# Optimization experiments

Measured on AMD Instinct MI355X. Metric: run time of the kernel, lower is better.

The kernel has to match this reference:

```python
import jax, jax.numpy as jnp
import numpy as np

IN_C = 256
INTER_C = 64  # in_c // k, k=4
B, H, W = 8, 32, 32
N_TERMS = 5   # numSeriesTerms; numTraceSamples = 1


def setup_inputs():
    key = jax.random.key(0)
    ks = jax.random.split(key, 10)
    s = 0.05
    return {
        "x": jax.random.normal(ks[0], (B, IN_C, H, W), jnp.float32),
        "Wq": jax.random.normal(ks[1], (INTER_C, IN_C), jnp.float32) * s,
        "bq": jax.random.normal(ks[2], (INTER_C,), jnp.float32) * s,
        "Wk": jax.random.normal(ks[3], (INTER_C, IN_C), jnp.float32) * s,
        "bk": jax.random.normal(ks[4], (INTER_C,), jnp.float32) * s,
        "Wc": jax.random.normal(ks[5], (2 * INTER_C,), jnp.float32) * s,
        "Wv": jax.random.normal(ks[6], (IN_C, IN_C), jnp.float32) * s,
        "bv": jax.random.normal(ks[7], (IN_C,), jnp.float32) * s,
        "gamma": jnp.full((1,), 0.5, jnp.float32),
        "u": jax.random.normal(ks[8], (B, IN_C, H, W), jnp.float32),
    }


def _attention(x, Wq, bq, Wk, bk, Wc, Wv, bv, gamma):
    # Attention_concat.forward. concat_conv is a bias-free linear map over the
    # channel concat, so energy[i,j] = <Wc[:ic], q_i> + <Wc[ic:], k_j> exactly.
    b, c, h, w = x.shape
    n = h * w
    xf = x.reshape(b, c, n)                                   # [B,C,N]
    q = jnp.einsum('oc,bcn->bon', Wq, xf) + bq[None, :, None]  # [B,ic,N]
    k = jnp.einsum('oc,bcn->bon', Wk, xf) + bk[None, :, None]  # [B,ic,N]
    ic = Wq.shape[0]
    eq = jnp.einsum('c,bcn->bn', Wc[:ic], q)                  # [B,N]
    ek = jnp.einsum('c,bcn->bn', Wc[ic:], k)                  # [B,N]
    attn = (eq[:, :, None] + ek[:, None, :]) / n              # energy/(H*W), [B,N,N]
    v = jnp.einsum('oc,bcn->bon', Wv, xf) + bv[None, :, None]  # [B,C,N]
    out = jnp.einsum('bcn,bnm->bcm', v, attn).reshape(b, c, h, w)
    return gamma * out + x


def _forward(x, Wq, bq, Wk, bk, Wc, Wv, bv, gamma, u):
    att = lambda z, g: _attention(z, Wq, bq, Wk, bk, Wc, Wv, bv, g)
    # turbulance_hook: runs under torch.no_grad and rescales gamma in-place
    res = att(x, gamma)
    turbu = att(x * 1.0000001, gamma)
    lip = jnp.linalg.norm(turbu - res) / jnp.linalg.norm(x * 1.0000001 - x)
    factor = jax.lax.stop_gradient(jnp.where(lip > 0.9, 0.9 / lip, 1.0))
    gamma_eff = gamma * factor
    Fx, vjp_fn = jax.vjp(lambda z: att(z, gamma_eff), x)
    # power_series_matrix_logarithm_trace: Hutchinson estimate of
    # tr(log(I+J)) ~= sum_j (-1)^{j+1}/j * u^T J^j u, 1 probe, 5 terms
    b = x.shape[0]
    uf = u.reshape(b, -1)
    vcur = u
    tr = jnp.zeros((b,), x.dtype)
    for j in range(1, N_TERMS + 1):
        vcur = vjp_fn(vcur)[0]                 # u^T J^j via repeated vjp
        dot = jnp.sum(vcur.reshape(b, -1) * uf, axis=1)
        tr = tr + ((-1.0) ** (j + 1) / j) * dot
    return x + Fx, tr


def reference(x, Wq, bq, Wk, bk, Wc, Wv, bv, gamma, u):
    return _forward(x, Wq, bq, Wk, bk, Wc, Wv, bv, gamma, u)
```

## Files before the change

kernel.cpp:

```cpp
#include <hip/hip_runtime.h>
#include <math.h>

#define NB 8
#define NC 256
#define NN 1024
#define NICH 64

#define WS_AQ    0
#define WS_AK    256
#define WS_MOM2  520
#define WS_SX    1024
#define WS_XE    3072
#define WS_XK    5120
#define WS_T1P   7424
#define WS_T2P   7488
#define WS_VSU   7680
#define WS_UE    9728
#define WS_VEU   11776
#define WS_CAQ   13824
#define WS_CAK   15872
#define WS_CUAK  17920
#define WS_STAT  20480
#define STAT_STRIDE 2560
#define ST_EK    1024
#define ST_SV    2048
#define ST_SVE   2304
#define WS_EQP2  57344
#define WS_EKP2  90112
#define WS_MAQP2 122880
#define WS_MAKP2 155648
#define WS_SX2P  188416
#define WS_UUP   188672
#define WS_WVB   188928

typedef short bf16x8 __attribute__((ext_vector_type(8)));
typedef float f32x4 __attribute__((ext_vector_type(4)));
union FragU { uint4 u; bf16x8 h; };

__device__ __forceinline__ float dot4(const float4& a, const float4& b) {
    return a.x * b.x + a.y * b.y + a.z * b.z + a.w * b.w;
}
__device__ __forceinline__ float sum4(const float4& a) {
    return a.x + a.y + a.z + a.w;
}
__device__ __forceinline__ unsigned int bf16lo(float v) {
    unsigned int u = __float_as_uint(v);
    return (u + 0x7FFFu + ((u >> 16) & 1u)) >> 16;
}
__device__ __forceinline__ unsigned int bf16hi(float v) {
    unsigned int u = __float_as_uint(v);
    return (u + 0x7FFFu + ((u >> 16) & 1u)) & 0xFFFF0000u;
}

__global__ void kA(const float* __restrict__ x, const float* __restrict__ u,
                   const float* __restrict__ Wq, const float* __restrict__ Wk,
                   const float* __restrict__ Wc, const float* __restrict__ Wv,
                   float* __restrict__ ws) {
    const int bid = blockIdx.x;
    const int t = threadIdx.x;
    __shared__ float tile[64][65];
    __shared__ float aql[64], akl[64];
    __shared__ float4 red_e[32][8], red_k[32][8], red_a[32][8], red_m[32][8];
    if (bid >= 256) {
        const int o0 = (bid - 256) * 64;
        const int cho = t >> 6, ol = t & 63;
        uint4* wvb4 = (uint4*)((unsigned int*)ws + WS_WVB);
        for (int p4 = 0; p4 < 4; ++p4) {
#pragma unroll 4
            for (int p = 0; p < 16; ++p) {
                int cl = p * 4 + cho;
                tile[cl][ol] = Wv[(size_t)(p4 * 64 + cl) * NC + o0 + ol];
            }
            __syncthreads();
#pragma unroll
            for (int i = 0; i < 2; ++i) {
                int idx2 = i * 256 + t;
                int o_l = idx2 >> 3, gg = idx2 & 7;
                int g = p4 * 8 + gg;
                int o = o0 + o_l;
                int s = g ^ (o & 7);
                uint4 outv;
                outv.x = bf16lo(tile[gg * 8 + 0][o_l]) | bf16hi(tile[gg * 8 + 1][o_l]);
                outv.y = bf16lo(tile[gg * 8 + 2][o_l]) | bf16hi(tile[gg * 8 + 3][o_l]);
                outv.z = bf16lo(tile[gg * 8 + 4][o_l]) | bf16hi(tile[gg * 8 + 5][o_l]);
                outv.w = bf16lo(tile[gg * 8 + 6][o_l]) | bf16hi(tile[gg * 8 + 7][o_l]);
                wvb4[(size_t)(bid - 256) * 2048 + o_l * 32 + s] = outv;
            }
            __syncthreads();
        }
        return;
    }
    const int b = bid >> 5, r = bid & 31;
    const int nq = r >> 2, chq = r & 3;
    if (t < 64) {
        const int c = chq * 64 + t;
        float a = 0.f, k = 0.f;
#pragma unroll 8
        for (int o = 0; o < 64; ++o) {
            a += Wc[o] * Wq[o * NC + c];
            k += Wc[64 + o] * Wk[o * NC + c];
        }
        aql[t] = a; akl[t] = k;
        if (nq == 0) { ws[WS_AQ + c] = a; ws[WS_AK + c] = k; }
    }
    __syncthreads();
    const int f4g = t & 31, sub = t >> 5;
    const float4* xb4 = (const float4*)(x + ((size_t)b * NC + chq * 64) * NN);
    const float4* ub4 = (const float4*)(u + ((size_t)b * NC + chq * 64) * NN);
    float4 eqp = {0.f, 0.f, 0.f, 0.f}, ekp = {0.f, 0.f, 0.f, 0.f};
    float4 map = {0.f, 0.f, 0.f, 0.f}, mkp = {0.f, 0.f, 0.f, 0.f};
#pragma unroll
    for (int i = 0; i < 8; ++i) {
        const int cl = sub * 8 + i;
        float4 xv = xb4[cl * 256 + nq * 32 + f4g];
        float4 uv = ub4[cl * 256 + nq * 32 + f4g];
        const float a = aql[cl], kk = akl[cl];
        eqp.x += a * xv.x;  eqp.y += a * xv.y;  eqp.z += a * xv.z;  eqp.w += a * xv.w;
        ekp.x += kk * xv.x; ekp.y += kk * xv.y; ekp.z += kk * xv.z; ekp.w += kk * xv.w;
        map.x += a * uv.x;  map.y += a * uv.y;  map.z += a * uv.z;  map.w += a * uv.w;
        mkp.x += kk * uv.x; mkp.y += kk * uv.y; mkp.z += kk * uv.z; mkp.w += kk * uv.w;
    }
    red_e[f4g][sub] = eqp; red_k[f4g][sub] = ekp;
    red_a[f4g][sub] = map; red_m[f4g][sub] = mkp;
    __syncthreads();
    if (t < 32) {
        float4 e = red_e[t][0], k = red_k[t][0], a = red_a[t][0], m = red_m[t][0];
#pragma unroll
        for (int s2 = 1; s2 < 8; ++s2) {
            float4 v;
            v = red_e[t][s2]; e.x += v.x; e.y += v.y; e.z += v.z; e.w += v.w;
            v = red_k[t][s2]; k.x += v.x; k.y += v.y; k.z += v.z; k.w += v.w;
            v = red_a[t][s2]; a.x += v.x; a.y += v.y; a.z += v.z; a.w += v.w;
            v = red_m[t][s2]; m.x += v.x; m.y += v.y; m.z += v.z; m.w += v.w;
        }
        const size_t po = (size_t)(b * 4 + chq) * 1024 + nq * 128;
        ((float4*)(ws + WS_EQP2  + po))[t] = e;
        ((float4*)(ws + WS_EKP2  + po))[t] = k;
        ((float4*)(ws + WS_MAQP2 + po))[t] = a;
        ((float4*)(ws + WS_MAKP2 + po))[t] = m;
    }
}

__global__ void kB(const float* __restrict__ x, const float* __restrict__ u,
                   const float* __restrict__ Wc, const float* __restrict__ bq,
                   const float* __restrict__ bk, float* __restrict__ ws) {
    const int bid = blockIdx.x;
    const int b = bid >> 5, g = bid & 31;
    const int c0 = g * 8;
    const int t = threadIdx.x;
    const int wid = t >> 6, lane = t & 63;
    __shared__ float s_cq, s_ck;
    __shared__ float mred[4][4];
    __shared__ float wv9[8][9][4];
    __shared__ float accw[2][4];
    if (t < 64) {
        float p = Wc[t] * bq[t], rr = Wc[64 + t] * bk[t];
        for (int off = 32; off > 0; off >>= 1) {
            p += __shfl_down(p, off, 64);
            rr += __shfl_down(rr, off, 64);
        }
        if (t == 0) { s_cq = p; s_ck = rr; }
    }
    __syncthreads();
    const float cq = s_cq, ck = s_ck;
    float4 e4 = {0.f, 0.f, 0.f, 0.f}, k4 = {0.f, 0.f, 0.f, 0.f};
    float4 ma4 = {0.f, 0.f, 0.f, 0.f}, mk4 = {0.f, 0.f, 0.f, 0.f};
#pragma unroll
    for (int q = 0; q < 4; ++q) {
        const size_t po = (size_t)(b * 4 + q) * 1024;
        float4 v;
        v = ((const float4*)(ws + WS_EQP2  + po))[t];
        e4.x += v.x; e4.y += v.y; e4.z += v.z; e4.w += v.w;
        v = ((const float4*)(ws + WS_EKP2  + po))[t];
        k4.x += v.x; k4.y += v.y; k4.z += v.z; k4.w += v.w;
        v = ((const float4*)(ws + WS_MAQP2 + po))[t];
        ma4.x += v.x; ma4.y += v.y; ma4.z += v.z; ma4.w += v.w;
        v = ((const float4*)(ws + WS_MAKP2 + po))[t];
        mk4.x += v.x; mk4.y += v.y; mk4.z += v.z; mk4.w += v.w;
    }
    e4.x += cq; e4.y += cq; e4.z += cq; e4.w += cq;
    k4.x += ck; k4.y += ck; k4.z += ck; k4.w += ck;
    {
        float d0 = sum4(e4), d1 = sum4(k4), d2 = dot4(k4, k4), d3 = dot4(e4, k4);
        for (int off = 32; off > 0; off >>= 1) {
            d0 += __shfl_down(d0, off, 64);
            d1 += __shfl_down(d1, off, 64);
            d2 += __shfl_down(d2, off, 64);
            d3 += __shfl_down(d3, off, 64);
        }
        if (lane == 0) { mred[0][wid] = d0; mred[1][wid] = d1; mred[2][wid] = d2; mred[3][wid] = d3; }
    }
    __syncthreads();
    if (t == 0)
        for (int m = 0; m < 4; ++m)
            ws[WS_MOM2 + b * 4 + m] = mred[m][0] + mred[m][1] + mred[m][2] + mred[m][3];
    if (g == 0)
        ((float4*)(ws + WS_STAT + b * STAT_STRIDE + ST_EK))[t] = k4;
    const float4* xb4 = (const float4*)(x + ((size_t)b * NC + c0) * NN);
    const float4* ub4 = (const float4*)(u + ((size_t)b * NC + c0) * NN);
    float x2a = 0.f, uua = 0.f;
#pragma unroll
    for (int c = 0; c < 8; ++c) {
        float4 xv = xb4[c * 256 + t];
        float4 uv = ub4[c * 256 + t];
        float d[9];
        d[0] = dot4(xv, e4);
        d[1] = dot4(xv, k4);
        d[2] = sum4(uv);
        d[3] = dot4(uv, e4);
        d[4] = dot4(uv, k4);
        d[5] = dot4(xv, ma4);
        d[6] = dot4(xv, mk4);
        d[7] = dot4(uv, mk4);
        d[8] = sum4(xv);
        x2a += dot4(xv, xv);
        uua += dot4(uv, uv);
        for (int off = 32; off > 0; off >>= 1)
            for (int m = 0; m < 9; ++m) d[m] += __shfl_down(d[m], off, 64);
        if (lane == 0) for (int m = 0; m < 9; ++m) wv9[c][m][wid] = d[m];
    }
    for (int off = 32; off > 0; off >>= 1) {
        x2a += __shfl_down(x2a, off, 64);
        uua += __shfl_down(uua, off, 64);
    }
    if (lane == 0) { accw[0][wid] = x2a; accw[1][wid] = uua; }
    __syncthreads();
    if (t < 8) {
        int c = t;
        float v[9];
        for (int m = 0; m < 9; ++m)
            v[m] = wv9[c][m][0] + wv9[c][m][1] + wv9[c][m][2] + wv9[c][m][3];
        ws[WS_XE   + b * NC + c0 + c] = v[0];
        ws[WS_XK   + b * NC + c0 + c] = v[1];
        ws[WS_VSU  + b * NC + c0 + c] = v[2];
        ws[WS_UE   + b * NC + c0 + c] = v[3];
        ws[WS_VEU  + b * NC + c0 + c] = v[4];
        ws[WS_CAQ  + b * NC + c0 + c] = v[5];
        ws[WS_CAK  + b * NC + c0 + c] = v[6];
        ws[WS_CUAK + b * NC + c0 + c] = v[7];
        ws[WS_SX   + b * NC + c0 + c] = v[8];
    }
    if (t == 0) {
        ws[WS_SX2P + bid] = accw[0][0] + accw[0][1] + accw[0][2] + accw[0][3];
        ws[WS_UUP + bid]  = accw[1][0] + accw[1][1] + accw[1][2] + accw[1][3];
    }
}

__global__ void ksv(const float* __restrict__ Wv, const float* __restrict__ bv,
                    const float* __restrict__ Wc, const float* __restrict__ bq,
                    const float* __restrict__ bk, float* __restrict__ ws) {
    const int bid = blockIdx.x;
    const int b = bid >> 3, oc = bid & 7;
    const int t = threadIdx.x;
    const int o_sub = t >> 3, ks = t & 7;
    const int o = oc * 32 + o_sub;
    __shared__ float sxl[NC], xel[NC];
    __shared__ float T1s[32], T2s[32];
    __shared__ float s_cq, s_ck;
    if (t < 64) {
        float p = Wc[t] * bq[t], rr = Wc[64 + t] * bk[t];
        for (int off = 32; off > 0; off >>= 1) {
            p += __shfl_down(p, off, 64);
            rr += __shfl_down(rr, off, 64);
        }
        if (t == 0) { s_cq = p; s_ck = rr; }
    }
    sxl[t] = ws[WS_SX + b * NC + t];
    xel[t] = ws[WS_XE + b * NC + t];
    __syncthreads();
    const float Seq  = ws[WS_MOM2 + b * 4 + 0];
    const float Sek  = ws[WS_MOM2 + b * 4 + 1];
    const float Sek2 = ws[WS_MOM2 + b * 4 + 2];
    const float cq = s_cq, ck = s_ck;
    float wsx = 0.f, wxe = 0.f;
    const float4* wrow = (const float4*)(Wv + (size_t)o * NC);
#pragma unroll
    for (int i = 0; i < 8; ++i) {
        float4 w4 = wrow[i * 8 + ks];
        int k = i * 32 + ks * 4;
        wsx += w4.x * sxl[k] + w4.y * sxl[k + 1] + w4.z * sxl[k + 2] + w4.w * sxl[k + 3];
        wxe += w4.x * xel[k] + w4.y * xel[k + 1] + w4.z * xel[k + 2] + w4.w * xel[k + 3];
    }
    for (int off = 4; off > 0; off >>= 1) {
        wsx += __shfl_down(wsx, off, 8);
        wxe += __shfl_down(wxe, off, 8);
    }
    if (ks == 0) {
        float bvc = bv[o];
        float Sv  = wsx + (float)NN * bvc;
        float SvL = wsx;
        float Sve = wxe + bvc * Seq;
        float* st = ws + WS_STAT + b * STAT_STRIDE;
        st[ST_SV + o] = Sv; st[ST_SVE + o] = Sve;
        float A = 2.f * Sve - bvc * Seq - cq * Sv;
        float sx = sxl[o];
        float xk = ws[WS_XK + b * NC + o];
        float xkL = xk - ck * sx;
        float T1c = A * sx + Sv * xkL + SvL * xk;
        float SP  = Sek - (float)NN * ck;
        float SP2 = Sek2 - 2.f * ck * Sek + (float)NN * ck * ck;
        float SPQ = Sek2 - ck * Sek;
        float T2c = (float)NN * A * A + Sv * Sv * SP2 + SvL * SvL * Sek2
                  + 2.f * A * Sv * SP + 2.f * A * SvL * Sek + 2.f * Sv * SvL * SPQ;
        T1s[o_sub] = T1c; T2s[o_sub] = T2c;
    }
    __syncthreads();
    if (t == 0) {
        float t1 = 0.f, t2 = 0.f;
        for (int i = 0; i < 32; ++i) { t1 += T1s[i]; t2 += T2s[i]; }
        ws[WS_T1P + bid] = t1;
        ws[WS_T2P + bid] = t2;
    }
}

struct KFSMem {
    unsigned int Wlds[32768];
    unsigned int Vsb[128] __attribute__((aligned(16)));
    unsigned int Veb[128] __attribute__((aligned(16)));
    float P_lds[256];
    float R_lds[256];
    float dred[9][4];
    float gred0[4];
    float gredT[2];
    float sge;
};

__global__ void __launch_bounds__(1024, 4) kfin(
        const float* __restrict__ x, const float* __restrict__ bv,
        const float* __restrict__ gamma, float* __restrict__ ws,
        float* __restrict__ out) {
    __shared__ __align__(16) unsigned char smem_raw[sizeof(KFSMem)];
    KFSMem& S = *(KFSMem*)smem_raw;
    const int bid = blockIdx.x;
    const int t = threadIdx.x;
    const int lane = t & 63;
    const bool is_iter = (bid < 8);
    uint4 stg0, stg1, stg2, stg3, stg4, stg5, stg6, stg7;
    if (is_iter) {
        const uint4* wvb4 = (const uint4*)((const unsigned int*)ws + WS_WVB);
        stg0 = wvb4[0 * 1024 + t]; stg1 = wvb4[1 * 1024 + t];
        stg2 = wvb4[2 * 1024 + t]; stg3 = wvb4[3 * 1024 + t];
        stg4 = wvb4[4 * 1024 + t]; stg5 = wvb4[5 * 1024 + t];
        stg6 = wvb4[6 * 1024 + t]; stg7 = wvb4[7 * 1024 + t];
    }
    {
        float a = 0.f, b1 = 0.f, c1 = 0.f;
        if (t < 256) a = ws[WS_SX2P + t];
        if (t < 64) { b1 = ws[WS_T1P + t]; c1 = ws[WS_T2P + t]; }
        for (int off = 32; off > 0; off >>= 1) {
            a  += __shfl_down(a,  off, 64);
            b1 += __shfl_down(b1, off, 64);
            c1 += __shfl_down(c1, off, 64);
        }
        if (t < 256 && lane == 0) S.gred0[t >> 6] = a;
        if (t == 0) { S.gredT[0] = b1; S.gredT[1] = c1; }
    }
    __syncthreads();
    if (t == 0) {
        float S1 = S.gred0[0] + S.gred0[1] + S.gred0[2] + S.gred0[3];
        float inv = gamma[0] * (1.f / (float)NN);
        float dd = S1 + 2.f * inv * S.gredT[0] + inv * inv * S.gredT[1];
        float lip = sqrtf(dd / S1);
        S.sge = gamma[0] * ((lip > 0.9f) ? (0.9f / lip) : 1.f);
    }
    __syncthreads();
    const float ge = S.sge;

    if (!is_iter) {
        const float gn = ge * (1.f / (float)NN);
        const int r = t >> 8, tc = t & 255;
        const int bid2 = (bid - 8) * 4 + r;
        const int b = bid2 >> 8, c = bid2 & 255;
        const float* st = ws + WS_STAT + b * STAT_STRIDE;
        float sv = st[ST_SV + c], sve = st[ST_SVE + c];
        float4 ek4 = ((const float4*)(st + ST_EK))[tc];
        size_t i4 = (size_t)bid2 * 256 + tc;
        float4 x4 = ((const float4*)x)[i4];
        float4 o;
        o.x = 2.f * x4.x + gn * (sve + ek4.x * sv);
        o.y = 2.f * x4.y + gn * (sve + ek4.y * sv);
        o.z = 2.f * x4.z + gn * (sve + ek4.z * sv);
        o.w = 2.f * x4.w + gn * (sve + ek4.w * sv);
        ((float4*)out)[i4] = o;
        return;
    }

    const int b = bid;
    const int nt = t >> 6;
    const int row = lane & 15;
    const int kgrp = lane >> 4;
    const int o = nt * 16 + row;
    const int wid4 = (t & 255) >> 6;
    ((uint4*)S.Wlds)[0 * 1024 + t] = stg0; ((uint4*)S.Wlds)[1 * 1024 + t] = stg1;
    ((uint4*)S.Wlds)[2 * 1024 + t] = stg2; ((uint4*)S.Wlds)[3 * 1024 + t] = stg3;
    ((uint4*)S.Wlds)[4 * 1024 + t] = stg4; ((uint4*)S.Wlds)[5 * 1024 + t] = stg5;
    ((uint4*)S.Wlds)[6 * 1024 + t] = stg6; ((uint4*)S.Wlds)[7 * 1024 + t] = stg7;
    const float s = ge * (1.f / (float)NN);
    float Svl_r = 0.f, sxl_r = 0.f, xkl_r = 0.f, caql_r = 0.f, cakl_r = 0.f,
          Uel_r = 0.f, Vsul_r = 0.f, bvl_r = 0.f, aql_r = 0.f, akl_r = 0.f,
          veu_r = 0.f, cuak_r = 0.f, vsreg = 0.f, vereg = 0.f;
    if (t < 256) {
        const float* st = ws + WS_STAT + b * STAT_STRIDE;
        Svl_r  = st[ST_SV + t];
        sxl_r  = ws[WS_SX   + b * NC + t];
        xkl_r  = ws[WS_XK   + b * NC + t];
        caql_r = ws[WS_CAQ  + b * NC + t];
        cakl_r = ws[WS_CAK  + b * NC + t];
        Uel_r  = ws[WS_UE   + b * NC + t];
        Vsul_r = ws[WS_VSU  + b * NC + t];
        veu_r  = ws[WS_VEU  + b * NC + t];
        cuak_r = ws[WS_CUAK + b * NC + t];
        aql_r  = ws[WS_AQ + t];
        akl_r  = ws[WS_AK + t];
        bvl_r  = bv[t];
        vsreg = Vsul_r; vereg = veu_r;
        float vs_o = __shfl_xor(vsreg, 1, 64);
        float ve_o = __shfl_xor(vereg, 1, 64);
        if ((t & 1) == 0) {
            S.Vsb[t >> 1] = bf16lo(vsreg) | bf16hi(vs_o);
            S.Veb[t >> 1] = bf16lo(vereg) | bf16hi(ve_o);
        }
    }
    const float Seq  = ws[WS_MOM2 + b * 4 + 0];
    const float Sek  = ws[WS_MOM2 + b * 4 + 1];
    const float Sekq = ws[WS_MOM2 + b * 4 + 3];
    float uu = 0.f;
    for (int g = 0; g < 32; ++g) uu += ws[WS_UUP + b * 32 + g];
    __syncthreads();
    if (t < 256) {
        float d[8] = {Svl_r * cuak_r, aql_r * Vsul_r, akl_r * Vsul_r, akl_r * Uel_r,
                      Svl_r * Vsul_r, Svl_r * veu_r,  Svl_r * aql_r,  Svl_r * akl_r};
        for (int off = 32; off > 0; off >>= 1)
            for (int m = 0; m < 8; ++m) d[m] += __shfl_down(d[m], off, 64);
        if (lane == 0) for (int m = 0; m < 8; ++m) S.dred[m][wid4] = d[m];
    }
    __syncthreads();
    float g2a = 0.f, aqVsu = 0.f, akVsu = 0.f, akUe = 0.f, SvVsu = 0.f, SvVeu = 0.f,
          Svaq = 0.f, Svak = 0.f;
    if (t < 256) {
        g2a   = S.dred[0][0] + S.dred[0][1] + S.dred[0][2] + S.dred[0][3];
        aqVsu = S.dred[1][0] + S.dred[1][1] + S.dred[1][2] + S.dred[1][3];
        akVsu = S.dred[2][0] + S.dred[2][1] + S.dred[2][2] + S.dred[2][3];
        akUe  = S.dred[3][0] + S.dred[3][1] + S.dred[3][2] + S.dred[3][3];
        SvVsu = S.dred[4][0] + S.dred[4][1] + S.dred[4][2] + S.dred[4][3];
        SvVeu = S.dred[5][0] + S.dred[5][1] + S.dred[5][2] + S.dred[5][3];
        Svaq  = S.dred[6][0] + S.dred[6][1] + S.dred[6][2] + S.dred[6][3];
        Svak  = S.dred[7][0] + S.dred[7][1] + S.dred[7][2] + S.dred[7][3];
    }
    __syncthreads();
    const float lam = 1.f + s * Svak;
    float alpha = 1.f, beta = 0.f, gam = 0.f;
    float SxAcc = 0.f, XkAcc = 0.f, CakAcc = 0.f;
    float dot = uu, tr = 0.f;
    const float coef[5] = {1.f, -0.5f, 1.f / 3.f, -0.25f, 0.2f};
    const uint4* Vsb4 = (const uint4*)S.Vsb;
    const uint4* Veb4 = (const uint4*)S.Veb;
    const uint4* Wlds4 = (const uint4*)S.Wlds;
    for (int j = 0; j < 5; ++j) {
        f32x4 acc = {0.f, 0.f, 0.f, 0.f};
#pragma unroll
        for (int kc = 0; kc < 8; ++kc) {
            const uint4* asrc = (row == 1) ? Veb4 : Vsb4;
            uint4 araw = asrc[kc * 4 + kgrp];
            if (row >= 2) { araw.x = 0u; araw.y = 0u; araw.z = 0u; araw.w = 0u; }
            FragU fa; fa.u = araw;
            FragU fb; fb.u = Wlds4[o * 32 + ((kc * 4 + kgrp) ^ (o & 7))];
            acc = __builtin_amdgcn_mfma_f32_16x16x32_bf16(fa.h, fb.h, acc, 0, 0, 0);
        }
        if (lane < 16) {
            S.P_lds[nt * 16 + lane] = acc[0];
            S.R_lds[nt * 16 + lane] = acc[1];
        }
        __syncthreads();
        if (t < 256) {
            float Pv = s * S.P_lds[t];
            float Rv = s * S.R_lds[t];
            float d[9];
            d[0] = Svl_r * Pv;
            d[1] = Svl_r * Rv;
            d[2] = bvl_r * vsreg;
            d[3] = sxl_r * Pv;
            d[4] = xkl_r * Pv;
            d[5] = caql_r * Pv;
            d[6] = cakl_r * Pv;
            d[7] = Uel_r * Pv;
            d[8] = Vsul_r * Rv;
            for (int off = 32; off > 0; off >>= 1)
                for (int m = 0; m < 9; ++m) d[m] += __shfl_down(d[m], off, 64);
            if (lane == 0) for (int m = 0; m < 9; ++m) S.dred[m][wid4] = d[m];
        }
        __syncthreads();
        if (t < 256) {
            float Pv = s * S.P_lds[t];
            float Rv = s * S.R_lds[t];
            float sm[9];
            for (int m = 0; m < 9; ++m)
                sm[m] = S.dred[m][0] + S.dred[m][1] + S.dred[m][2] + S.dred[m][3];
            const float svP = sm[0], svR = sm[1], bvVs = sm[2], sxP = sm[3], xkP = sm[4],
                        caqP = sm[5], cakP = sm[6], ueP = sm[7], vsuR = sm[8];
            const float sB = s * bvVs;
            float St  = s * (alpha * SvVsu + beta * (float)NN + gam * Seq  + Svaq * SxAcc);
            float tek = s * (alpha * SvVeu + beta * Sek        + gam * Sekq + Svaq * XkAcc);
            float uta = s * (alpha * g2a   + beta * akVsu      + gam * akUe + Svaq * CakAcc);
            dot += ueP + caqP + sB * aqVsu + uta + vsuR;
            tr  += coef[j] * dot;
            float nVs = vsreg + Pv * Seq  + aql_r * (sxP + (float)NN * sB) + akl_r * St  + Rv * (float)NN;
            float nVe = vereg + Pv * Sekq + aql_r * (xkP + sB * Sek)       + akl_r * tek + Rv * Sek;
            vsreg = nVs; vereg = nVe;
            float vs_o = __shfl_xor(nVs, 1, 64);
            float ve_o = __shfl_xor(nVe, 1, 64);
            if ((t & 1) == 0) {
                S.Vsb[t >> 1] = bf16lo(nVs) | bf16hi(vs_o);
                S.Veb[t >> 1] = bf16lo(nVe) | bf16hi(ve_o);
            }
            SxAcc  = lam * SxAcc  + sxP;
            XkAcc  = lam * XkAcc  + xkP;
            CakAcc = lam * CakAcc + cakP;
            beta = lam * beta + Svaq * sB + svR;
            gam  = lam * gam + svP;
            alpha *= lam;
        }
        __syncthreads();
    }
    if (t == 0) out[2097152 + b] = tr;
}

extern "C" void kernel_launch(void* const* d_in, const int* in_sizes, int n_in,
                              void* d_out, int out_size, void* d_ws, size_t ws_size,
                              hipStream_t stream) {
    const float* x     = (const float*)d_in[0];
    const float* Wq    = (const float*)d_in[1];
    const float* bq    = (const float*)d_in[2];
    const float* Wk    = (const float*)d_in[3];
    const float* bk    = (const float*)d_in[4];
    const float* Wc    = (const float*)d_in[5];
    const float* Wv    = (const float*)d_in[6];
    const float* bv    = (const float*)d_in[7];
    const float* gamma = (const float*)d_in[8];
    const float* u     = (const float*)d_in[9];
    float* out = (float*)d_out;
    float* ws  = (float*)d_ws;

    kA  <<<dim3(260), dim3(256),  0, stream>>>(x, u, Wq, Wk, Wc, Wv, ws);
    kB  <<<dim3(256), dim3(256),  0, stream>>>(x, u, Wc, bq, bk, ws);
    ksv <<<dim3(64),  dim3(256),  0, stream>>>(Wv, bv, Wc, bq, bk, ws);
    kfin<<<dim3(520), dim3(1024), 0, stream>>>(x, bv, gamma, ws, out);
}
```

Baseline: 45.31 us.

## Fuse kA and kB into one pass with per-column-tile partial statistics

Merges the two preprocessing kernels into a single kernel. Each block stages a 256-channel by 32-column tile of x and u in shared memory, computes eq and ek for its columns, and then writes 11 per-channel partial sums to workspace. The final reductions of those partials, along with the moments of eq and ek, now happen in ksv and kfin. This removes one launch and the second full read of x and u. In exchange, ksv and kfin must read and reduce a larger partial buffer, and the tile staging uses strided 32-float loads.

```diff
diff --git a/kernel.cpp b/kernel.cpp
--- a/kernel.cpp
+++ b/kernel.cpp
@@ -9,40 +9,23 @@
 #define WS_AQ    0
 #define WS_AK    256
 #define WS_MOM2  520
-#define WS_SX    1024
-#define WS_XE    3072
-#define WS_XK    5120
+#define WS_SX2B  552
 #define WS_T1P   7424
 #define WS_T2P   7488
-#define WS_VSU   7680
-#define WS_UE    9728
-#define WS_VEU   11776
-#define WS_CAQ   13824
-#define WS_CAK   15872
-#define WS_CUAK  17920
 #define WS_STAT  20480
 #define STAT_STRIDE 2560
+#define ST_EQ    0
 #define ST_EK    1024
 #define ST_SV    2048
 #define ST_SVE   2304
-#define WS_EQP2  57344
-#define WS_EKP2  90112
-#define WS_MAQP2 122880
-#define WS_MAKP2 155648
-#define WS_SX2P  188416
-#define WS_UUP   188672
-#define WS_WVB   188928
+#define WS_P11   57344
+#define P11_AS   65536
+#define WS_WVB   778240
 
 typedef short bf16x8 __attribute__((ext_vector_type(8)));
 typedef float f32x4 __attribute__((ext_vector_type(4)));
 union FragU { uint4 u; bf16x8 h; };
 
-__device__ __forceinline__ float dot4(const float4& a, const float4& b) {
-    return a.x * b.x + a.y * b.y + a.z * b.z + a.w * b.w;
-}
-__device__ __forceinline__ float sum4(const float4& a) {
-    return a.x + a.y + a.z + a.w;
-}
 __device__ __forceinline__ unsigned int bf16lo(float v) {
     unsigned int u = __float_as_uint(v);
     return (u + 0x7FFFu + ((u >> 16) & 1u)) >> 16;
@@ -52,16 +35,21 @@
     return (u + 0x7FFFu + ((u >> 16) & 1u)) & 0xFFFF0000u;
 }
 
-__global__ void kA(const float* __restrict__ x, const float* __restrict__ u,
-                   const float* __restrict__ Wq, const float* __restrict__ Wk,
+__global__ void kP(const float* __restrict__ x, const float* __restrict__ u,
+                   const float* __restrict__ Wq, const float* __restrict__ bq,
+                   const float* __restrict__ Wk, const float* __restrict__ bk,
                    const float* __restrict__ Wc, const float* __restrict__ Wv,
                    float* __restrict__ ws) {
     const int bid = blockIdx.x;
     const int t = threadIdx.x;
-    __shared__ float tile[64][65];
-    __shared__ float aql[64], akl[64];
-    __shared__ float4 red_e[32][8], red_k[32][8], red_a[32][8], red_m[32][8];
+    __shared__ float tile_x[256][33];
+    __shared__ float tile_u[256][33];
+    __shared__ float aql[256], akl[256];
+    __shared__ float eq_l[32], ek_l[32], maq_l[32], mak_l[32];
+    __shared__ float red4[4][8][32];
+    __shared__ float s_cq, s_ck;
     if (bid >= 256) {
+        float (*tile)[65] = (float(*)[65])&tile_x[0][0];
         const int o0 = (bid - 256) * 64;
         const int cho = t >> 6, ol = t & 63;
         uint4* wvb4 = (uint4*)((unsigned int*)ws + WS_WVB);
@@ -90,69 +78,17 @@
         }
         return;
     }
-    const int b = bid >> 5, r = bid & 31;
-    const int nq = r >> 2, chq = r & 3;
-    if (t < 64) {
-        const int c = chq * 64 + t;
+    const int b = bid >> 5, nc = bid & 31;
+    {
         float a = 0.f, k = 0.f;
 #pragma unroll 8
         for (int o = 0; o < 64; ++o) {
-            a += Wc[o] * Wq[o * NC + c];
-            k += Wc[64 + o] * Wk[o * NC + c];
+            a += Wc[o] * Wq[o * NC + t];
+            k += Wc[64 + o] * Wk[o * NC + t];
         }
         aql[t] = a; akl[t] = k;
-        if (nq == 0) { ws[WS_AQ + c] = a; ws[WS_AK + c] = k; }
-    }
-    __syncthreads();
-    const int f4g = t & 31, sub = t >> 5;
-    const float4* xb4 = (const float4*)(x + ((size_t)b * NC + chq * 64) * NN);
-    const float4* ub4 = (const float4*)(u + ((size_t)b * NC + chq * 64) * NN);
-    float4 eqp = {0.f, 0.f, 0.f, 0.f}, ekp = {0.f, 0.f, 0.f, 0.f};
-    float4 map = {0.f, 0.f, 0.f, 0.f}, mkp = {0.f, 0.f, 0.f, 0.f};
-#pragma unroll
-    for (int i = 0; i < 8; ++i) {
-        const int cl = sub * 8 + i;
-        float4 xv = xb4[cl * 256 + nq * 32 + f4g];
-        float4 uv = ub4[cl * 256 + nq * 32 + f4g];
-        const float a = aql[cl], kk = akl[cl];
-        eqp.x += a * xv.x;  eqp.y += a * xv.y;  eqp.z += a * xv.z;  eqp.w += a * xv.w;
-        ekp.x += kk * xv.x; ekp.y += kk * xv.y; ekp.z += kk * xv.z; ekp.w += kk * xv.w;
-        map.x += a * uv.x;  map.y += a * uv.y;  map.z += a * uv.z;  map.w += a * uv.w;
-        mkp.x += kk * uv.x; mkp.y += kk * uv.y; mkp.z += kk * uv.z; mkp.w += kk * uv.w;
-    }
-    red_e[f4g][sub] = eqp; red_k[f4g][sub] = ekp;
-    red_a[f4g][sub] = map; red_m[f4g][sub] = mkp;
-    __syncthreads();
-    if (t < 32) {
-        float4 e = red_e[t][0], k = red_k[t][0], a = red_a[t][0], m = red_m[t][0];
-#pragma unroll
-        for (int s2 = 1; s2 < 8; ++s2) {
-            float4 v;
-            v = red_e[t][s2]; e.x += v.x; e.y += v.y; e.z += v.z; e.w += v.w;
-            v = red_k[t][s2]; k.x += v.x; k.y += v.y; k.z += v.z; k.w += v.w;
-            v = red_a[t][s2]; a.x += v.x; a.y += v.y; a.z += v.z; a.w += v.w;
-            v = red_m[t][s2]; m.x += v.x; m.y += v.y; m.z += v.z; m.w += v.w;
-        }
-        const size_t po = (size_t)(b * 4 + chq) * 1024 + nq * 128;
-        ((float4*)(ws + WS_EQP2  + po))[t] = e;
-        ((float4*)(ws + WS_EKP2  + po))[t] = k;
-        ((float4*)(ws + WS_MAQP2 + po))[t] = a;
-        ((float4*)(ws + WS_MAKP2 + po))[t] = m;
-    }
-}
-
-__global__ void kB(const float* __restrict__ x, const float* __restrict__ u,
-                   const float* __restrict__ Wc, const float* __restrict__ bq,
-                   const float* __restrict__ bk, float* __restrict__ ws) {
-    const int bid = blockIdx.x;
-    const int b = bid >> 5, g = bid & 31;
-    const int c0 = g * 8;
-    const int t = threadIdx.x;
-    const int wid = t >> 6, lane = t & 63;
-    __shared__ float s_cq, s_ck;
-    __shared__ float mred[4][4];
-    __shared__ float wv9[8][9][4];
-    __shared__ float accw[2][4];
+        if (nc == 0) { ws[WS_AQ + t] = a; ws[WS_AK + t] = k; }
+    }
     if (t < 64) {
         float p = Wc[t] * bq[t], rr = Wc[64 + t] * bk[t];
         for (int off = 32; off > 0; off >>= 1) {
@@ -161,88 +97,71 @@
         }
         if (t == 0) { s_cq = p; s_ck = rr; }
     }
-    __syncthreads();
-    const float cq = s_cq, ck = s_ck;
-    float4 e4 = {0.f, 0.f, 0.f, 0.f}, k4 = {0.f, 0.f, 0.f, 0.f};
-    float4 ma4 = {0.f, 0.f, 0.f, 0.f}, mk4 = {0.f, 0.f, 0.f, 0.f};
-#pragma unroll
-    for (int q = 0; q < 4; ++q) {
-        const size_t po = (size_t)(b * 4 + q) * 1024;
-        float4 v;
-        v = ((const float4*)(ws + WS_EQP2  + po))[t];
-        e4.x += v.x; e4.y += v.y; e4.z += v.z; e4.w += v.w;
-        v = ((const float4*)(ws + WS_EKP2  + po))[t];
-        k4.x += v.x; k4.y += v.y; k4.z += v.z; k4.w += v.w;
-        v = ((const float4*)(ws + WS_MAQP2 + po))[t];
-        ma4.x += v.x; ma4.y += v.y; ma4.z += v.z; ma4.w += v.w;
-        v = ((const float4*)(ws + WS_MAKP2 + po))[t];
-        mk4.x += v.x; mk4.y += v.y; mk4.z += v.z; mk4.w += v.w;
-    }
-    e4.x += cq; e4.y += cq; e4.z += cq; e4.w += cq;
-    k4.x += ck; k4.y += ck; k4.z += ck; k4.w += ck;
-    {
-        float d0 = sum4(e4), d1 = sum4(k4), d2 = dot4(k4, k4), d3 = dot4(e4, k4);
-        for (int off = 32; off > 0; off >>= 1) {
-            d0 += __shfl_down(d0, off, 64);
-            d1 += __shfl_down(d1, off, 64);
-            d2 += __shfl_down(d2, off, 64);
-            d3 += __shfl_down(d3, off, 64);
-        }
-        if (lane == 0) { mred[0][wid] = d0; mred[1][wid] = d1; mred[2][wid] = d2; mred[3][wid] = d3; }
-    }
-    __syncthreads();
-    if (t == 0)
-        for (int m = 0; m < 4; ++m)
-            ws[WS_MOM2 + b * 4 + m] = mred[m][0] + mred[m][1] + mred[m][2] + mred[m][3];
-    if (g == 0)
-        ((float4*)(ws + WS_STAT + b * STAT_STRIDE + ST_EK))[t] = k4;
-    const float4* xb4 = (const float4*)(x + ((size_t)b * NC + c0) * NN);
-    const float4* ub4 = (const float4*)(u + ((size_t)b * NC + c0) * NN);
-    float x2a = 0.f, uua = 0.f;
-#pragma unroll
-    for (int c = 0; c < 8; ++c) {
-        float4 xv = xb4[c * 256 + t];
-        float4 uv = ub4[c * 256 + t];
-        float d[9];
-        d[0] = dot4(xv, e4);
-        d[1] = dot4(xv, k4);
-        d[2] = sum4(uv);
-        d[3] = dot4(uv, e4);
-        d[4] = dot4(uv, k4);
-        d[5] = dot4(xv, ma4);
-        d[6] = dot4(xv, mk4);
-        d[7] = dot4(uv, mk4);
-        d[8] = sum4(xv);
-        x2a += dot4(xv, xv);
-        uua += dot4(uv, uv);
-        for (int off = 32; off > 0; off >>= 1)
-            for (int m = 0; m < 9; ++m) d[m] += __shfl_down(d[m], off, 64);
-        if (lane == 0) for (int m = 0; m < 9; ++m) wv9[c][m][wid] = d[m];
-    }
-    for (int off = 32; off > 0; off >>= 1) {
-        x2a += __shfl_down(x2a, off, 64);
-        uua += __shfl_down(uua, off, 64);
-    }
-    if (lane == 0) { accw[0][wid] = x2a; accw[1][wid] = uua; }
-    __syncthreads();
-    if (t < 8) {
-        int c = t;
-        float v[9];
-        for (int m = 0; m < 9; ++m)
-            v[m] = wv9[c][m][0] + wv9[c][m][1] + wv9[c][m][2] + wv9[c][m][3];
-        ws[WS_XE   + b * NC + c0 + c] = v[0];
-        ws[WS_XK   + b * NC + c0 + c] = v[1];
-        ws[WS_VSU  + b * NC + c0 + c] = v[2];
-        ws[WS_UE   + b * NC + c0 + c] = v[3];
-        ws[WS_VEU  + b * NC + c0 + c] = v[4];
-        ws[WS_CAQ  + b * NC + c0 + c] = v[5];
-        ws[WS_CAK  + b * NC + c0 + c] = v[6];
-        ws[WS_CUAK + b * NC + c0 + c] = v[7];
-        ws[WS_SX   + b * NC + c0 + c] = v[8];
-    }
-    if (t == 0) {
-        ws[WS_SX2P + bid] = accw[0][0] + accw[0][1] + accw[0][2] + accw[0][3];
-        ws[WS_UUP + bid]  = accw[1][0] + accw[1][1] + accw[1][2] + accw[1][3];
+    const float* xb = x + (size_t)b * NC * NN + nc * 32;
+    const float* ub = u + (size_t)b * NC * NN + nc * 32;
+    {
+        const int cs = t >> 5, nl = t & 31;
+#pragma unroll 8
+        for (int r2 = 0; r2 < 32; ++r2) {
+            int c = r2 * 8 + cs;
+            tile_x[c][nl] = xb[(size_t)c * NN + nl];
+            tile_u[c][nl] = ub[(size_t)c * NN + nl];
+        }
+    }
+    __syncthreads();
+    {
+        const int nl = t & 31, grp = t >> 5;
+        float ea = 0.f, ka = 0.f, ma = 0.f, mk = 0.f;
+#pragma unroll 8
+        for (int i = 0; i < 32; ++i) {
+            int c = grp * 32 + i;
+            float xv = tile_x[c][nl], uv = tile_u[c][nl];
+            float a = aql[c], kk = akl[c];
+            ea += a * xv; ka += kk * xv;
+            ma += a * uv; mk += kk * uv;
+        }
+        red4[0][grp][nl] = ea; red4[1][grp][nl] = ka;
+        red4[2][grp][nl] = ma; red4[3][grp][nl] = mk;
+    }
+    __syncthreads();
+    if (t < 32) {
+        float e = 0.f, k = 0.f, m = 0.f, mq = 0.f;
+#pragma unroll
+        for (int g = 0; g < 8; ++g) {
+            e += red4[0][g][t]; k += red4[1][g][t];
+            m += red4[2][g][t]; mq += red4[3][g][t];
+        }
+        e += s_cq; k += s_ck;
+        eq_l[t] = e; ek_l[t] = k; maq_l[t] = m; mak_l[t] = mq;
+        float* st = ws + WS_STAT + b * STAT_STRIDE;
+        st[ST_EQ + nc * 32 + t] = e;
+        st[ST_EK + nc * 32 + t] = k;
+    }
+    __syncthreads();
+    {
+        float acc[11];
+#pragma unroll
+        for (int a2 = 0; a2 < 11; ++a2) acc[a2] = 0.f;
+#pragma unroll 8
+        for (int n = 0; n < 32; ++n) {
+            float xv = tile_x[t][n], uv = tile_u[t][n];
+            float e = eq_l[n], kk = ek_l[n], m = maq_l[n], mq = mak_l[n];
+            acc[0] += xv;
+            acc[1] += xv * e;
+            acc[2] += xv * kk;
+            acc[3] += uv;
+            acc[4] += uv * e;
+            acc[5] += uv * kk;
+            acc[6] += xv * m;
+            acc[7] += xv * mq;
+            acc[8] += uv * mq;
+            acc[9] += xv * xv;
+            acc[10] += uv * uv;
+        }
+        const int idx = (b * 32 + nc) * 256 + t;
+#pragma unroll
+        for (int a2 = 0; a2 < 11; ++a2)
+            ws[WS_P11 + a2 * P11_AS + idx] = acc[a2];
     }
 }
 
@@ -252,10 +171,12 @@
     const int bid = blockIdx.x;
     const int b = bid >> 3, oc = bid & 7;
     const int t = threadIdx.x;
+    const int wid = t >> 6, lane = t & 63;
     const int o_sub = t >> 3, ks = t & 7;
     const int o = oc * 32 + o_sub;
-    __shared__ float sxl[NC], xel[NC];
+    __shared__ float sxl[NC], xel[NC], xkl[NC];
     __shared__ float T1s[32], T2s[32];
+    __shared__ float mred[5][4];
     __shared__ float s_cq, s_ck;
     if (t < 64) {
         float p = Wc[t] * bq[t], rr = Wc[64 + t] * bk[t];
@@ -265,12 +186,50 @@
         }
         if (t == 0) { s_cq = p; s_ck = rr; }
     }
-    sxl[t] = ws[WS_SX + b * NC + t];
-    xel[t] = ws[WS_XE + b * NC + t];
-    __syncthreads();
-    const float Seq  = ws[WS_MOM2 + b * 4 + 0];
-    const float Sek  = ws[WS_MOM2 + b * 4 + 1];
-    const float Sek2 = ws[WS_MOM2 + b * 4 + 2];
+    {
+        float sxa = 0.f, xea = 0.f, xka = 0.f, x2a = 0.f;
+#pragma unroll 8
+        for (int ncc = 0; ncc < 32; ++ncc) {
+            const int idx = (b * 32 + ncc) * 256 + t;
+            sxa += ws[WS_P11 + 0 * P11_AS + idx];
+            xea += ws[WS_P11 + 1 * P11_AS + idx];
+            xka += ws[WS_P11 + 2 * P11_AS + idx];
+            if (oc == 0) x2a += ws[WS_P11 + 9 * P11_AS + idx];
+        }
+        sxl[t] = sxa; xel[t] = xea; xkl[t] = xka;
+        if (oc == 0) {
+            for (int off = 32; off > 0; off >>= 1) x2a += __shfl_down(x2a, off, 64);
+            if (lane == 0) mred[4][wid] = x2a;
+        }
+    }
+    {
+        const float* st = ws + WS_STAT + b * STAT_STRIDE;
+        float4 e4 = ((const float4*)(st + ST_EQ))[t];
+        float4 k4 = ((const float4*)(st + ST_EK))[t];
+        float d0 = e4.x + e4.y + e4.z + e4.w;
+        float d1 = k4.x + k4.y + k4.z + k4.w;
+        float d2 = k4.x * k4.x + k4.y * k4.y + k4.z * k4.z + k4.w * k4.w;
+        float d3 = e4.x * k4.x + e4.y * k4.y + e4.z * k4.z + e4.w * k4.w;
+        for (int off = 32; off > 0; off >>= 1) {
+            d0 += __shfl_down(d0, off, 64);
+            d1 += __shfl_down(d1, off, 64);
+            d2 += __shfl_down(d2, off, 64);
+            d3 += __shfl_down(d3, off, 64);
+        }
+        if (lane == 0) { mred[0][wid] = d0; mred[1][wid] = d1; mred[2][wid] = d2; mred[3][wid] = d3; }
+    }
+    __syncthreads();
+    const float Seq  = mred[0][0] + mred[0][1] + mred[0][2] + mred[0][3];
+    const float Sek  = mred[1][0] + mred[1][1] + mred[1][2] + mred[1][3];
+    const float Sek2 = mred[2][0] + mred[2][1] + mred[2][2] + mred[2][3];
+    const float Sekq = mred[3][0] + mred[3][1] + mred[3][2] + mred[3][3];
+    if (oc == 0 && t == 0) {
+        ws[WS_MOM2 + b * 4 + 0] = Seq;
+        ws[WS_MOM2 + b * 4 + 1] = Sek;
+        ws[WS_MOM2 + b * 4 + 2] = Sek2;
+        ws[WS_MOM2 + b * 4 + 3] = Sekq;
+        ws[WS_SX2B + b] = mred[4][0] + mred[4][1] + mred[4][2] + mred[4][3];
+    }
     const float cq = s_cq, ck = s_ck;
     float wsx = 0.f, wxe = 0.f;
     const float4* wrow = (const float4*)(Wv + (size_t)o * NC);
@@ -294,7 +253,7 @@
         st[ST_SV + o] = Sv; st[ST_SVE + o] = Sve;
         float A = 2.f * Sve - bvc * Seq - cq * Sv;
         float sx = sxl[o];
-        float xk = ws[WS_XK + b * NC + o];
+        float xk = xkl[o];
         float xkL = xk - ck * sx;
         float T1c = A * sx + Sv * xkL + SvL * xk;
         float SP  = Sek - (float)NN * ck;
@@ -320,8 +279,7 @@
     float P_lds[256];
     float R_lds[256];
     float dred[9][4];
-    float gred0[4];
-    float gredT[2];
+    float redu[16];
     float sge;
 };
 
@@ -345,23 +303,19 @@
     }
     {
         float a = 0.f, b1 = 0.f, c1 = 0.f;
-        if (t < 256) a = ws[WS_SX2P + t];
+        if (t < 8) a = ws[WS_SX2B + t];
         if (t < 64) { b1 = ws[WS_T1P + t]; c1 = ws[WS_T2P + t]; }
         for (int off = 32; off > 0; off >>= 1) {
             a  += __shfl_down(a,  off, 64);
             b1 += __shfl_down(b1, off, 64);
             c1 += __shfl_down(c1, off, 64);
         }
-        if (t < 256 && lane == 0) S.gred0[t >> 6] = a;
-        if (t == 0) { S.gredT[0] = b1; S.gredT[1] = c1; }
-    }
-    __syncthreads();
-    if (t == 0) {
-        float S1 = S.gred0[0] + S.gred0[1] + S.gred0[2] + S.gred0[3];
-        float inv = gamma[0] * (1.f / (float)NN);
-        float dd = S1 + 2.f * inv * S.gredT[0] + inv * inv * S.gredT[1];
-        float lip = sqrtf(dd / S1);
-        S.sge = gamma[0] * ((lip > 0.9f) ? (0.9f / lip) : 1.f);
+        if (t == 0) {
+            float inv = gamma[0] * (1.f / (float)NN);
+            float dd = a + 2.f * inv * b1 + inv * inv * c1;
+            float lip = sqrtf(dd / a);
+            S.sge = gamma[0] * ((lip > 0.9f) ? (0.9f / lip) : 1.f);
+        }
     }
     __syncthreads();
     const float ge = S.sge;
@@ -391,29 +345,52 @@
     const int kgrp = lane >> 4;
     const int o = nt * 16 + row;
     const int wid4 = (t & 255) >> 6;
-    ((uint4*)S.Wlds)[0 * 1024 + t] = stg0; ((uint4*)S.Wlds)[1 * 1024 + t] = stg1;
-    ((uint4*)S.Wlds)[2 * 1024 + t] = stg2; ((uint4*)S.Wlds)[3 * 1024 + t] = stg3;
-    ((uint4*)S.Wlds)[4 * 1024 + t] = stg4; ((uint4*)S.Wlds)[5 * 1024 + t] = stg5;
-    ((uint4*)S.Wlds)[6 * 1024 + t] = stg6; ((uint4*)S.Wlds)[7 * 1024 + t] = stg7;
+    float* redq = (float*)S.Wlds;
+    {
+        const int c = t & 255, q = t >> 8;
+        float r8[8];
+#pragma unroll
+        for (int a2 = 0; a2 < 8; ++a2) r8[a2] = 0.f;
+        float uup = 0.f;
+#pragma unroll
+        for (int n2 = 0; n2 < 8; ++n2) {
+            const int idx = (b * 32 + q * 8 + n2) * 256 + c;
+            r8[0] += ws[WS_P11 + 0 * P11_AS + idx];
+            r8[1] += ws[WS_P11 + 2 * P11_AS + idx];
+            r8[2] += ws[WS_P11 + 3 * P11_AS + idx];
+            r8[3] += ws[WS_P11 + 4 * P11_AS + idx];
+            r8[4] += ws[WS_P11 + 5 * P11_AS + idx];
+            r8[5] += ws[WS_P11 + 6 * P11_AS + idx];
+            r8[6] += ws[WS_P11 + 7 * P11_AS + idx];
+            r8[7] += ws[WS_P11 + 8 * P11_AS + idx];
+            uup   += ws[WS_P11 + 10 * P11_AS + idx];
+        }
+#pragma unroll
+        for (int a2 = 0; a2 < 8; ++a2) redq[q * 2048 + a2 * 256 + c] = r8[a2];
+        for (int off = 32; off > 0; off >>= 1) uup += __shfl_down(uup, off, 64);
+        if (lane == 0) S.redu[t >> 6] = uup;
+    }
+    __syncthreads();
     const float s = ge * (1.f / (float)NN);
     float Svl_r = 0.f, sxl_r = 0.f, xkl_r = 0.f, caql_r = 0.f, cakl_r = 0.f,
           Uel_r = 0.f, Vsul_r = 0.f, bvl_r = 0.f, aql_r = 0.f, akl_r = 0.f,
           veu_r = 0.f, cuak_r = 0.f, vsreg = 0.f, vereg = 0.f;
+    float uu = 0.f;
     if (t < 256) {
+        float f[8];
+#pragma unroll
+        for (int a2 = 0; a2 < 8; ++a2)
+            f[a2] = redq[0 * 2048 + a2 * 256 + t] + redq[1 * 2048 + a2 * 256 + t]
+                  + redq[2 * 2048 + a2 * 256 + t] + redq[3 * 2048 + a2 * 256 + t];
+        sxl_r = f[0]; xkl_r = f[1]; Vsul_r = f[2]; Uel_r = f[3];
+        veu_r = f[4]; caql_r = f[5]; cakl_r = f[6]; cuak_r = f[7];
         const float* st = ws + WS_STAT + b * STAT_STRIDE;
-        Svl_r  = st[ST_SV + t];
-        sxl_r  = ws[WS_SX   + b * NC + t];
-        xkl_r  = ws[WS_XK   + b * NC + t];
-        caql_r = ws[WS_CAQ  + b * NC + t];
-        cakl_r = ws[WS_CAK  + b * NC + t];
-        Uel_r  = ws[WS_UE   + b * NC + t];
-        Vsul_r = ws[WS_VSU  + b * NC + t];
-        veu_r  = ws[WS_VEU  + b * NC + t];
-        cuak_r = ws[WS_CUAK + b * NC + t];
-        aql_r  = ws[WS_AQ + t];
-        akl_r  = ws[WS_AK + t];
-        bvl_r  = bv[t];
+        Svl_r = st[ST_SV + t];
+        aql_r = ws[WS_AQ + t];
+        akl_r = ws[WS_AK + t];
+        bvl_r = bv[t];
         vsreg = Vsul_r; vereg = veu_r;
+        for (int g = 0; g < 16; ++g) uu += S.redu[g];
         float vs_o = __shfl_xor(vsreg, 1, 64);
         float ve_o = __shfl_xor(vereg, 1, 64);
         if ((t & 1) == 0) {
@@ -424,9 +401,11 @@
     const float Seq  = ws[WS_MOM2 + b * 4 + 0];
     const float Sek  = ws[WS_MOM2 + b * 4 + 1];
     const float Sekq = ws[WS_MOM2 + b * 4 + 3];
-    float uu = 0.f;
-    for (int g = 0; g < 32; ++g) uu += ws[WS_UUP + b * 32 + g];
-    __syncthreads();
+    __syncthreads();
+    ((uint4*)S.Wlds)[0 * 1024 + t] = stg0; ((uint4*)S.Wlds)[1 * 1024 + t] = stg1;
+    ((uint4*)S.Wlds)[2 * 1024 + t] = stg2; ((uint4*)S.Wlds)[3 * 1024 + t] = stg3;
+    ((uint4*)S.Wlds)[4 * 1024 + t] = stg4; ((uint4*)S.Wlds)[5 * 1024 + t] = stg5;
+    ((uint4*)S.Wlds)[6 * 1024 + t] = stg6; ((uint4*)S.Wlds)[7 * 1024 + t] = stg7;
     if (t < 256) {
         float d[8] = {Svl_r * cuak_r, aql_r * Vsul_r, akl_r * Vsul_r, akl_r * Uel_r,
                       Svl_r * Vsul_r, Svl_r * veu_r,  Svl_r * aql_r,  Svl_r * akl_r};
@@ -541,8 +520,7 @@
     float* out = (float*)d_out;
     float* ws  = (float*)d_ws;
 
-    kA  <<<dim3(260), dim3(256),  0, stream>>>(x, u, Wq, Wk, Wc, Wv, ws);
-    kB  <<<dim3(256), dim3(256),  0, stream>>>(x, u, Wc, bq, bk, ws);
+    kP  <<<dim3(260), dim3(256),  0, stream>>>(x, u, Wq, bq, Wk, bk, Wc, Wv, ws);
     ksv <<<dim3(64),  dim3(256),  0, stream>>>(Wv, bv, Wc, bq, bk, ws);
     kfin<<<dim3(520), dim3(1024), 0, stream>>>(x, bv, gamma, ws, out);
 }
```

After: 53.70 us. +18.5%, slower.
